# Performance work log

Measured on AMD Instinct MI355X. Metric: run time of the kernel, lower is better.

The kernel has to match this reference:

```python
import jax, jax.numpy as jnp
import numpy as np

B, T, IN, H, K = 128, 4096, 2, 64, 2  # batch, seq_len, input feat, lstm hidden, num tags


def setup_inputs() -> dict:
    key = jax.random.key(0)
    ks = jax.random.split(key, 16)
    s = 1.0 / np.sqrt(H)
    u = lambda k, shape, a: jax.random.uniform(k, shape, jnp.float32, -a, a)
    p = {}
    p['x'] = jax.random.normal(ks[0], (B, T, IN), jnp.float32)
    # layer 0 (input IN), layer 1 (input 2H); leading dim 2 = [forward, backward] direction
    p['w_ih0'] = u(ks[1], (2, 4 * H, IN), s)
    p['w_hh0'] = u(ks[2], (2, 4 * H, H), s)
    p['b_ih0'] = u(ks[3], (2, 4 * H), s)
    p['b_hh0'] = u(ks[4], (2, 4 * H), s)
    p['w_ih1'] = u(ks[5], (2, 4 * H, 2 * H), s)
    p['w_hh1'] = u(ks[6], (2, 4 * H, H), s)
    p['b_ih1'] = u(ks[7], (2, 4 * H), s)
    p['b_hh1'] = u(ks[8], (2, 4 * H), s)
    p['fc_w'] = u(ks[9], (K, 2 * H), 1.0 / np.sqrt(2 * H))
    p['fc_b'] = u(ks[10], (K,), 1.0 / np.sqrt(2 * H))
    # CRF params (torchcrf init: U(-0.1, 0.1))
    p['trans'] = u(ks[11], (K, K), 0.1)
    p['start'] = u(ks[12], (K,), 0.1)
    p['end'] = u(ks[13], (K,), 0.1)
    return p


def _lstm_dir(xg, w_hh, b_hh):
    # xg: [T, B, 4H] precomputed input projections; PyTorch gate order i, f, g, o
    b, h = xg.shape[1], w_hh.shape[1]

    def step(carry, g_x):
        hs, cs = carry
        g = g_x + hs @ w_hh.T + b_hh
        i, f, gg, o = jnp.split(g, 4, axis=-1)
        cs = jax.nn.sigmoid(f) * cs + jax.nn.sigmoid(i) * jnp.tanh(gg)
        hs = jax.nn.sigmoid(o) * jnp.tanh(cs)
        return (hs, cs), hs

    init = (jnp.zeros((b, h), xg.dtype), jnp.zeros((b, h), xg.dtype))
    _, out = jax.lax.scan(step, init, xg)
    return out  # [T, B, H]


def _bilstm_layer(xt, w_ih, w_hh, b_ih, b_hh):
    # xt: [T, B, F] time-major input
    xg_f = jnp.einsum('tbi,gi->tbg', xt, w_ih[0]) + b_ih[0]
    xg_b = jnp.einsum('tbi,gi->tbg', xt[::-1], w_ih[1]) + b_ih[1]
    hf = _lstm_dir(xg_f, w_hh[0], b_hh[0])
    hb = _lstm_dir(xg_b, w_hh[1], b_hh[1])[::-1]
    return jnp.concatenate([hf, hb], axis=-1)  # [T, B, 2H]


def _viterbi(logits, trans, start, end):
    # logits: [B, T, K] -> best path [B, T]
    e = jnp.swapaxes(logits, 0, 1)  # [T, B, K]
    score0 = start[None, :] + e[0]

    def fwd(score, e_t):
        cand = score[:, :, None] + trans[None, :, :]  # [B, Kprev, Knext]
        bp = jnp.argmax(cand, axis=1)
        return jnp.max(cand, axis=1) + e_t, bp

    score, bps = jax.lax.scan(fwd, score0, e[1:])  # bps: [T-1, B, K]
    last = jnp.argmax(score + end[None, :], axis=-1)  # [B]

    def back(tag, bp):
        prev = jnp.take_along_axis(bp, tag[:, None], axis=1)[:, 0]
        return prev, prev

    _, path = jax.lax.scan(back, last, bps, reverse=True)  # [T-1, B]
    return jnp.swapaxes(jnp.concatenate([path, last[None, :]], axis=0), 0, 1)


def reference(x, w_ih0, w_hh0, b_ih0, b_hh0, w_ih1, w_hh1, b_ih1, b_hh1,
              fc_w, fc_b, trans, start, end):
    xt = jnp.swapaxes(x, 0, 1)  # [T, B, IN]
    h0 = _bilstm_layer(xt, w_ih0, w_hh0, b_ih0, b_hh0)
    h1 = _bilstm_layer(h0, w_ih1, w_hh1, b_ih1, b_hh1)  # [T, B, 2H]
    logits = jnp.swapaxes(jnp.einsum('tbh,kh->tbk', h1, fc_w) + fc_b, 0, 1)  # [B, T, K]
    return _viterbi(logits, trans, start, end).astype(jnp.int32)
```

## Files before the change

kernel.cpp:

```cpp
#include <hip/hip_runtime.h>
#include <hip/hip_bf16.h>

#define TT 4096
#define BATCH 128
#define HID 64
#define CK 32
#define NCH (TT / CK)
#define NSLOT (NCH + 1)

__device__ __forceinline__ float sigm(float x) { return 1.f / (1.f + expf(-x)); }
__device__ __forceinline__ float tanh_f(float x) { float e = expf(2.f * x); return 1.f - 2.f / (e + 1.f); }

__global__ __launch_bounds__(256, 1) void lstm_ckpt(
    const float* __restrict__ x,
    const float* __restrict__ w_ih,
    const float* __restrict__ w_hh,
    const float* __restrict__ b_ih, const float* __restrict__ b_hh,
    float* __restrict__ ckpt)
{
    const int blk = blockIdx.x;
    const int dir = blk & 1;
    const int b   = blk >> 1;
    const int tid = threadIdx.x;

    __shared__ __align__(16) float xs[TT * 2];
    __shared__ __align__(16) float h_lds[HID];
    __shared__ __align__(16) float g_lds[256];

    {
        const float4* src = (const float4*)(x + (size_t)b * TT * 2);
        float4* dst = (float4*)xs;
        #pragma unroll
        for (int r = 0; r < 8; ++r) dst[tid + r * 256] = src[tid + r * 256];
    }
    const int row = dir * 256 + tid;
    float wv[HID];
    {
        const float4* wr = (const float4*)(w_hh + (size_t)row * HID);
        #pragma unroll
        for (int k = 0; k < 16; ++k) {
            float4 v = wr[k];
            wv[4*k] = v.x; wv[4*k+1] = v.y; wv[4*k+2] = v.z; wv[4*k+3] = v.w;
        }
    }
    const float wx0 = w_ih[row * 2 + 0], wx1 = w_ih[row * 2 + 1];
    const float bias = b_ih[row] + b_hh[row];
    const int gtype = tid >> 6;
    float c = 0.f, hreg = 0.f;
    if (tid < HID) h_lds[tid] = 0.f;
    __syncthreads();

    for (int t = 0; t < TT; ++t) {
        const int tt = dir ? (TT - 1 - t) : t;
        if (tid < HID) {
            const int bnum = dir ? (tt + 1) : tt;
            if ((bnum & (CK - 1)) == 0) {
                float* cp = ckpt + (((size_t)(dir * BATCH + b) * NSLOT + (bnum >> 5)) << 7);
                cp[tid] = hreg; cp[HID + tid] = c;
            }
        }
        const float base = bias + wx0 * xs[tt * 2] + wx1 * xs[tt * 2 + 1];
        float a0 = 0.f, a1 = 0.f, a2 = 0.f, a3 = 0.f;
        const float4* h4 = (const float4*)h_lds;
        #pragma unroll
        for (int k = 0; k < 16; ++k) {
            float4 hv = h4[k];
            a0 = fmaf(wv[4*k],   hv.x, a0);
            a1 = fmaf(wv[4*k+1], hv.y, a1);
            a2 = fmaf(wv[4*k+2], hv.z, a2);
            a3 = fmaf(wv[4*k+3], hv.w, a3);
        }
        const float acc = base + ((a0 + a1) + (a2 + a3));
        g_lds[tid] = (gtype == 2) ? tanh_f(acc) : sigm(acc);
        __syncthreads();
        if (tid < HID) {
            const float iv = g_lds[tid], fv = g_lds[64 + tid], gg = g_lds[128 + tid], ov = g_lds[192 + tid];
            c = fv * c + iv * gg;
            hreg = ov * tanh_f(c);
            h_lds[tid] = hreg;
        }
        __syncthreads();
    }
}

__global__ __launch_bounds__(1024) void lstm_fused1(
    const float* __restrict__ x,
    const float* __restrict__ w_ih0, const float* __restrict__ w_hh0,
    const float* __restrict__ b_ih0, const float* __restrict__ b_hh0,
    const float* __restrict__ w_ih1, const float* __restrict__ w_hh1,
    const float* __restrict__ b_ih1, const float* __restrict__ b_hh1,
    const float* __restrict__ fc_w,  const float* __restrict__ ckpt,
    float* __restrict__ plog)
{
    const int blk = blockIdx.x;
    const int l1dir = blk & 1;
    const int b = blk >> 1;
    const int tid = threadIdx.x;

    __shared__ __align__(16) float h0buf[2][CK][128];
    __shared__ __align__(16) float xbuf[2][CK][2];
    __shared__ __align__(16) float g1[256];
    __shared__ __align__(16) float g0[2][256];
    __shared__ __align__(16) float h1_lds[HID];
    __shared__ __align__(16) float h0s[2][HID];

    const bool isL1 = (tid < 512);
    const int l1row = tid >> 1;
    const int l1half = tid & 1;
    const int d0 = (tid >> 8) - 2;
    const int st0 = tid & 255;

    float wreg[96];
    float bias_, fw0 = 0.f, fw1 = 0.f;
    int gtype_;
    float c_state = 0.f, ckh = 0.f, ckc = 0.f;
    float4 xpre = make_float4(0.f, 0.f, 0.f, 0.f);

    if (isL1) {
        const int grow = l1dir * 256 + l1row;
        const float* wi = w_ih1 + (size_t)grow * 128;
        const float* wh = w_hh1 + (size_t)grow * 64;
        const float4* srcA = (const float4*)wi + (l1half ? 24 : 0);
        const float4* srcB = l1half ? (const float4*)wh : ((const float4*)wi + 8);
        #pragma unroll
        for (int k = 0; k < 8; ++k) {
            float4 v = srcA[k];
            wreg[4*k] = v.x; wreg[4*k+1] = v.y; wreg[4*k+2] = v.z; wreg[4*k+3] = v.w;
        }
        #pragma unroll
        for (int k = 0; k < 16; ++k) {
            float4 v = srcB[k];
            wreg[32+4*k] = v.x; wreg[32+4*k+1] = v.y; wreg[32+4*k+2] = v.z; wreg[32+4*k+3] = v.w;
        }
        bias_ = b_ih1[grow] + b_hh1[grow];
        gtype_ = l1row >> 6;
    } else {
        const int growd = d0 * 256 + st0;
        const float4* wh = (const float4*)(w_hh0 + (size_t)growd * 64);
        #pragma unroll
        for (int k = 0; k < 16; ++k) {
            float4 v = wh[k];
            wreg[4*k] = v.x; wreg[4*k+1] = v.y; wreg[4*k+2] = v.z; wreg[4*k+3] = v.w;
        }
        wreg[64] = w_ih0[growd * 2 + 0];
        wreg[65] = w_ih0[growd * 2 + 1];
        bias_ = b_ih0[growd] + b_hh0[growd];
        gtype_ = st0 >> 6;
        if (d0 == 1 && st0 >= 64 && st0 < 128) {
            fw0 = fc_w[l1dir * 64 + (st0 - 64)];
            fw1 = fc_w[128 + l1dir * 64 + (st0 - 64)];
        }
    }

    if (tid < HID) h1_lds[tid] = 0.f;
    {
        const int ch0 = l1dir ? (NCH - 1) : 0;
        if (tid < 16)
            ((float4*)xbuf[0])[tid] = ((const float4*)(x + ((size_t)b * TT + (size_t)ch0 * CK) * 2))[tid];
        if (!isL1 && st0 < HID) {
            const int slot = d0 ? (ch0 + 1) : ch0;
            const float* cp = ckpt + (((size_t)(d0 * BATCH + b) * NSLOT + slot) << 7);
            h0s[d0][st0] = cp[st0];
            c_state = cp[HID + st0];
        }
    }
    __syncthreads();

    auto stepf = [&](int s, int ml, int mc, int mp) {
        if (s == 0 && mp >= 0 && !isL1) {
            const int chp = l1dir ? (NCH - 1 - mp) : mp;
            if (st0 < HID) {
                const int slot = d0 ? (chp + 1) : chp;
                const float* cp = ckpt + (((size_t)(d0 * BATCH + b) * NSLOT + slot) << 7);
                ckh = cp[st0]; ckc = cp[HID + st0];
            }
            if (d0 == 1 && st0 >= 128 && st0 < 144)
                xpre = ((const float4*)(x + ((size_t)b * TT + (size_t)chp * CK) * 2))[st0 - 128];
        }
        if (isL1) {
            if (ml >= 0) {
                const int trow = l1dir ? (CK - 1 - s) : s;
                const float* h0row = h0buf[ml & 1][trow];
                const float4* pA = (const float4*)h0row + (l1half ? 24 : 0);
                const float4* pB = l1half ? (const float4*)h1_lds : ((const float4*)h0row + 8);
                float a0 = 0.f, a1 = 0.f, a2 = 0.f, a3 = 0.f;
                #pragma unroll
                for (int k = 0; k < 8; ++k) {
                    float4 v = pA[k];
                    a0 = fmaf(wreg[4*k],   v.x, a0);
                    a1 = fmaf(wreg[4*k+1], v.y, a1);
                    a2 = fmaf(wreg[4*k+2], v.z, a2);
                    a3 = fmaf(wreg[4*k+3], v.w, a3);
                }
                #pragma unroll
                for (int k = 0; k < 16; ++k) {
                    float4 v = pB[k];
                    a0 = fmaf(wreg[32+4*k],   v.x, a0);
                    a1 = fmaf(wreg[32+4*k+1], v.y, a1);
                    a2 = fmaf(wreg[32+4*k+2], v.z, a2);
                    a3 = fmaf(wreg[32+4*k+3], v.w, a3);
                }
                float tot = (a0 + a1) + (a2 + a3);
                tot += __shfl_xor(tot, 1);
                tot += bias_;
                const float gv = (gtype_ == 2) ? tanh_f(tot) : sigm(tot);
                if (l1half == 0) g1[l1row] = gv;
            }
        } else {
            if (mc >= 0) {
                const int r0 = d0 ? (CK - 1 - s) : s;
                const float4* hsrc = (const float4*)h0s[d0];
                float a0 = 0.f, a1 = 0.f, a2 = 0.f, a3 = 0.f;
                #pragma unroll
                for (int k = 0; k < 16; ++k) {
                    float4 v = hsrc[k];
                    a0 = fmaf(wreg[4*k],   v.x, a0);
                    a1 = fmaf(wreg[4*k+1], v.y, a1);
                    a2 = fmaf(wreg[4*k+2], v.z, a2);
                    a3 = fmaf(wreg[4*k+3], v.w, a3);
                }
                float tot = (a0 + a1) + (a2 + a3) + bias_
                          + wreg[64] * xbuf[mc & 1][r0][0] + wreg[65] * xbuf[mc & 1][r0][1];
                const float gv = (gtype_ == 2) ? tanh_f(tot) : sigm(tot);
                g0[d0][st0] = gv;
            }
            if (d0 == 1 && st0 >= 64 && st0 < 128 && ml >= 0) {
                const int gt = ml * CK + s;
                if (gt > 0) {
                    const int l = st0 - 64;
                    const float hv = h1_lds[l];
                    float p0 = hv * fw0, p1 = hv * fw1;
                    #pragma unroll
                    for (int d_ = 32; d_ > 0; d_ >>= 1) { p0 += __shfl_xor(p0, d_); p1 += __shfl_xor(p1, d_); }
                    if (l == 0) {
                        const int tp = l1dir ? (TT - gt) : (gt - 1);
                        *(float2*)(plog + (((size_t)l1dir * BATCH + b) * TT + tp) * 2) = make_float2(p0, p1);
                    }
                }
            }
        }
        __syncthreads();
        if (isL1) {
            if (ml >= 0 && tid < HID) {
                const float iv = g1[tid], fv = g1[64 + tid], gg = g1[128 + tid], ov = g1[192 + tid];
                c_state = fv * c_state + iv * gg;
                h1_lds[tid] = ov * tanh_f(c_state);
            }
        } else {
            if (mc >= 0 && st0 < HID) {
                const float iv = g0[d0][st0], fv = g0[d0][64 + st0], gg = g0[d0][128 + st0], ov = g0[d0][192 + st0];
                c_state = fv * c_state + iv * gg;
                const float hv = ov * tanh_f(c_state);
                const int orow = d0 ? (CK - 1 - s) : s;
                h0buf[mc & 1][orow][d0 * HID + st0] = hv;
                if (s == CK - 1 && mp >= 0) { h0s[d0][st0] = ckh; c_state = ckc; }
                else h0s[d0][st0] = hv;
            }
            if (s == CK - 1 && mp >= 0 && d0 == 1 && st0 >= 128 && st0 < 144)
                ((float4*)xbuf[mp & 1])[st0 - 128] = xpre;
        }
        __syncthreads();
    };

    for (int s = 0; s < CK; ++s) stepf(s, -1, 0, 1);
    for (int i = 0; i < NCH; ++i) {
        const int mc = (i + 1 < NCH) ? (i + 1) : -1;
        const int mp = (i + 2 < NCH) ? (i + 2) : -1;
        for (int s = 0; s < CK; ++s) stepf(s, i, mc, mp);
    }
    if (!isL1 && d0 == 1 && st0 >= 64 && st0 < 128) {
        const int l = st0 - 64;
        const float hv = h1_lds[l];
        float p0 = hv * fw0, p1 = hv * fw1;
        #pragma unroll
        for (int d_ = 32; d_ > 0; d_ >>= 1) { p0 += __shfl_xor(p0, d_); p1 += __shfl_xor(p1, d_); }
        if (l == 0) {
            const int tp = l1dir ? 0 : (TT - 1);
            *(float2*)(plog + (((size_t)l1dir * BATCH + b) * TT + tp) * 2) = make_float2(p0, p1);
        }
    }
}

__device__ __forceinline__ unsigned long long shfl_u64(unsigned long long v, int src) {
    unsigned int lo = (unsigned int)v, hi = (unsigned int)(v >> 32);
    lo = __shfl(lo, src); hi = __shfl(hi, src);
    return ((unsigned long long)hi << 32) | lo;
}

__global__ __launch_bounds__(64, 1) void viterbi_k(
    const float* __restrict__ plog, const float* __restrict__ fc_b,
    const float* __restrict__ trans, const float* __restrict__ startv,
    const float* __restrict__ endv, int* __restrict__ out)
{
    const int b = blockIdx.x;
    const int lane = threadIdx.x;
    __shared__ __align__(16) float2 e_lds[64][65];

    const float fb0 = fc_b[0], fb1 = fc_b[1];
    const float* pf = plog + ((size_t)(0 * BATCH + b) * TT) * 2;
    const float* pb = plog + ((size_t)(1 * BATCH + b) * TT) * 2;
    for (int r = 0; r < 32; ++r) {
        const int i4 = r * 64 + lane;
        float4 a = ((const float4*)pf)[i4];
        float4 cc = ((const float4*)pb)[i4];
        const int t0 = 2 * i4, t1 = t0 + 1;
        e_lds[t0 & 63][t0 >> 6] = make_float2(a.x + cc.x + fb0, a.y + cc.y + fb1);
        e_lds[t1 & 63][t1 >> 6] = make_float2(a.z + cc.z + fb0, a.w + cc.w + fb1);
    }
    __syncthreads();
    const float tr00 = trans[0], tr01 = trans[1], tr10 = trans[2], tr11 = trans[3];
    const float2 e0 = e_lds[0][0];
    const float s00 = startv[0] + e0.x, s01 = startv[1] + e0.y;

    const int lo = lane * 64;
    const int hi = (lane == 63) ? (TT - 1) : (lo + 64);
    float a00, a01, a10, a11;
    {
        const float2 ee = e_lds[(lo + 1) & 63][(lo + 1) >> 6];
        a00 = tr00 + ee.x; a01 = tr01 + ee.y; a10 = tr10 + ee.x; a11 = tr11 + ee.y;
    }
    for (int t = lo + 2; t <= hi; ++t) {
        const float2 ee = e_lds[t & 63][t >> 6];
        const float n00 = fmaxf(a00 + tr00, a01 + tr10) + ee.x;
        const float n01 = fmaxf(a00 + tr01, a01 + tr11) + ee.y;
        const float n10 = fmaxf(a10 + tr00, a11 + tr10) + ee.x;
        const float n11 = fmaxf(a10 + tr01, a11 + tr11) + ee.y;
        a00 = n00; a01 = n01; a10 = n10; a11 = n11;
    }
    #pragma unroll
    for (int d = 1; d < 64; d <<= 1) {
        const float o00 = __shfl_up(a00, d), o01 = __shfl_up(a01, d);
        const float o10 = __shfl_up(a10, d), o11 = __shfl_up(a11, d);
        if (lane >= d) {
            const float n00 = fmaxf(o00 + a00, o01 + a10);
            const float n01 = fmaxf(o00 + a01, o01 + a11);
            const float n10 = fmaxf(o10 + a00, o11 + a10);
            const float n11 = fmaxf(o10 + a01, o11 + a11);
            a00 = n00; a01 = n01; a10 = n10; a11 = n11;
        }
    }
    const float p00 = __shfl_up(a00, 1), p01 = __shfl_up(a01, 1);
    const float p10 = __shfl_up(a10, 1), p11 = __shfl_up(a11, 1);
    float s0, s1;
    if (lane == 0) { s0 = s00; s1 = s01; }
    else { s0 = fmaxf(s00 + p00, s01 + p10); s1 = fmaxf(s00 + p01, s01 + p11); }
    unsigned long long m0 = 0ull, m1 = 0ull;
    for (int t = lo + 1; t <= hi; ++t) {
        const float2 ee = e_lds[t & 63][t >> 6];
        const float c00 = s0 + tr00, c10 = s1 + tr10;
        const float c01 = s0 + tr01, c11 = s1 + tr11;
        const int bp0 = c10 > c00, bp1 = c11 > c01;
        s0 = (bp0 ? c10 : c00) + ee.x;
        s1 = (bp1 ? c11 : c01) + ee.y;
        m0 |= (unsigned long long)bp0 << (t - lo - 1);
        m1 |= (unsigned long long)bp1 << (t - lo - 1);
    }
    int last;
    {
        const int lt = (s1 + endv[1]) > (s0 + endv[0]);
        last = __shfl(lt, 63);
    }
    int f0 = 0, f1 = 1;
    for (int t = hi; t > lo; --t) {
        const int s_ = t - lo - 1;
        f0 = (int)(((f0 ? m1 : m0) >> s_) & 1ull);
        f1 = (int)(((f1 ? m1 : m0) >> s_) & 1ull);
    }
    int mm = f0 | (f1 << 1);
    #pragma unroll
    for (int d = 1; d < 64; d <<= 1) {
        const int mo = __shfl_down(mm, d);
        if (lane + d < 64) {
            const int r0 = (mm >> (mo & 1)) & 1;
            const int r1 = (mm >> ((mo >> 1) & 1)) & 1;
            mm = r0 | (r1 << 1);
        }
    }
    const int gn = __shfl_down(mm, 1);
    int cur = (lane == 63) ? last : ((gn >> last) & 1);
    unsigned long long tagm = 0ull;
    if (lane == 63) tagm |= (unsigned long long)last << 63;
    for (int t = hi; t > lo; --t) {
        const int s_ = t - lo - 1;
        cur = (int)(((cur ? m1 : m0) >> s_) & 1ull);
        tagm |= (unsigned long long)cur << s_;
    }
    int* ob = out + (size_t)b * TT;
    for (int r = 0; r < 64; ++r) {
        const unsigned long long mr = shfl_u64(tagm, r);
        ob[r * 64 + lane] = (int)((mr >> lane) & 1ull);
    }
}

extern "C" void kernel_launch(void* const* d_in, const int* in_sizes, int n_in,
                              void* d_out, int out_size, void* d_ws, size_t ws_size,
                              hipStream_t stream) {
    const float* x      = (const float*)d_in[0];
    const float* w_ih0  = (const float*)d_in[1];
    const float* w_hh0  = (const float*)d_in[2];
    const float* b_ih0  = (const float*)d_in[3];
    const float* b_hh0  = (const float*)d_in[4];
    const float* w_ih1  = (const float*)d_in[5];
    const float* w_hh1  = (const float*)d_in[6];
    const float* b_ih1  = (const float*)d_in[7];
    const float* b_hh1  = (const float*)d_in[8];
    const float* fc_w   = (const float*)d_in[9];
    const float* fc_b   = (const float*)d_in[10];
    const float* trans  = (const float*)d_in[11];
    const float* startv = (const float*)d_in[12];
    const float* endv   = (const float*)d_in[13];

    char* ws = (char*)d_ws;
    const size_t ckpt_bytes = (size_t)2 * BATCH * NSLOT * 128 * 4;
    float* ckpt = (float*)ws;
    float* plog = (float*)(ws + ckpt_bytes);

    lstm_ckpt<<<256, 256, 0, stream>>>(x, w_ih0, w_hh0, b_ih0, b_hh0, ckpt);
    lstm_fused1<<<256, 1024, 0, stream>>>(x, w_ih0, w_hh0, b_ih0, b_hh0,
                                          w_ih1, w_hh1, b_ih1, b_hh1,
                                          fc_w, ckpt, plog);
    viterbi_k<<<128, 64, 0, stream>>>(plog, fc_b, trans, startv, endv, (int*)d_out);
}
```

Before: 8.068 ms.

## Halve fused LSTM block to 512 threads with two gate rows per thread

```diff
diff --git a/kernel.cpp b/kernel.cpp
--- a/kernel.cpp
+++ b/kernel.cpp
@@ -83,7 +83,7 @@
     }
 }
 
-__global__ __launch_bounds__(1024) void lstm_fused1(
+__global__ __launch_bounds__(512, 2) void lstm_fused1(
     const float* __restrict__ x,
     const float* __restrict__ w_ih0, const float* __restrict__ w_hh0,
     const float* __restrict__ b_ih0, const float* __restrict__ b_hh0,
@@ -101,163 +101,169 @@
     __shared__ __align__(16) float xbuf[2][CK][2];
     __shared__ __align__(16) float g1[256];
     __shared__ __align__(16) float g0[2][256];
-    __shared__ __align__(16) float h1_lds[HID];
+    __shared__ __align__(16) float h1b[2][HID];
     __shared__ __align__(16) float h0s[2][HID];
 
-    const bool isL1 = (tid < 512);
-    const int l1row = tid >> 1;
-    const int l1half = tid & 1;
-    const int d0 = (tid >> 8) - 2;
-    const int st0 = tid & 255;
-
-    float wreg[96];
-    float bias_, fw0 = 0.f, fw1 = 0.f;
-    int gtype_;
-    float c_state = 0.f, ckh = 0.f, ckc = 0.f;
+    const bool isL1 = (tid < 256);
+    const int t0 = tid - 256;
+    const int dg = t0 >> 7;
+    const int jg = t0 & 127;
+    const int du = t0 >> 6;
+    const int eu = t0 & 63;
+
+    float wreg[192];
+    float bias0 = 0.f, bias1 = 0.f;
+    float fw0 = 0.f, fw1 = 0.f;
+    float c_st = 0.f;
+    float ckh = 0.f, ckc = 0.f;
     float4 xpre = make_float4(0.f, 0.f, 0.f, 0.f);
 
     if (isL1) {
-        const int grow = l1dir * 256 + l1row;
-        const float* wi = w_ih1 + (size_t)grow * 128;
-        const float* wh = w_hh1 + (size_t)grow * 64;
-        const float4* srcA = (const float4*)wi + (l1half ? 24 : 0);
-        const float4* srcB = l1half ? (const float4*)wh : ((const float4*)wi + 8);
-        #pragma unroll
-        for (int k = 0; k < 8; ++k) {
-            float4 v = srcA[k];
+        const int grow = l1dir * 256 + tid;
+        const float4* wia = (const float4*)(w_ih1 + (size_t)grow * 128);
+        #pragma unroll
+        for (int k = 0; k < 32; ++k) {
+            float4 v = wia[k];
             wreg[4*k] = v.x; wreg[4*k+1] = v.y; wreg[4*k+2] = v.z; wreg[4*k+3] = v.w;
         }
+        const float4* wha = (const float4*)(w_hh1 + (size_t)grow * 64);
         #pragma unroll
         for (int k = 0; k < 16; ++k) {
-            float4 v = srcB[k];
-            wreg[32+4*k] = v.x; wreg[32+4*k+1] = v.y; wreg[32+4*k+2] = v.z; wreg[32+4*k+3] = v.w;
-        }
-        bias_ = b_ih1[grow] + b_hh1[grow];
-        gtype_ = l1row >> 6;
+            float4 v = wha[k];
+            wreg[128+4*k] = v.x; wreg[128+4*k+1] = v.y; wreg[128+4*k+2] = v.z; wreg[128+4*k+3] = v.w;
+        }
+        bias0 = b_ih1[grow] + b_hh1[grow];
     } else {
-        const int growd = d0 * 256 + st0;
-        const float4* wh = (const float4*)(w_hh0 + (size_t)growd * 64);
+        const int rA = dg * 256 + jg;
+        const int rB = rA + 128;
+        const float4* wa = (const float4*)(w_hh0 + (size_t)rA * 64);
+        const float4* wb = (const float4*)(w_hh0 + (size_t)rB * 64);
         #pragma unroll
         for (int k = 0; k < 16; ++k) {
-            float4 v = wh[k];
+            float4 v = wa[k];
             wreg[4*k] = v.x; wreg[4*k+1] = v.y; wreg[4*k+2] = v.z; wreg[4*k+3] = v.w;
         }
-        wreg[64] = w_ih0[growd * 2 + 0];
-        wreg[65] = w_ih0[growd * 2 + 1];
-        bias_ = b_ih0[growd] + b_hh0[growd];
-        gtype_ = st0 >> 6;
-        if (d0 == 1 && st0 >= 64 && st0 < 128) {
-            fw0 = fc_w[l1dir * 64 + (st0 - 64)];
-            fw1 = fc_w[128 + l1dir * 64 + (st0 - 64)];
-        }
-    }
-
-    if (tid < HID) h1_lds[tid] = 0.f;
+        #pragma unroll
+        for (int k = 0; k < 16; ++k) {
+            float4 v = wb[k];
+            wreg[64+4*k] = v.x; wreg[64+4*k+1] = v.y; wreg[64+4*k+2] = v.z; wreg[64+4*k+3] = v.w;
+        }
+        wreg[128] = w_ih0[rA * 2 + 0]; wreg[129] = w_ih0[rA * 2 + 1];
+        wreg[130] = w_ih0[rB * 2 + 0]; wreg[131] = w_ih0[rB * 2 + 1];
+        bias0 = b_ih0[rA] + b_hh0[rA];
+        bias1 = b_ih0[rB] + b_hh0[rB];
+        if (t0 >= 128 && t0 < 192) {
+            fw0 = fc_w[l1dir * 64 + (t0 - 128)];
+            fw1 = fc_w[128 + l1dir * 64 + (t0 - 128)];
+        }
+    }
+
+    if (tid < HID) { h1b[0][tid] = 0.f; h1b[1][tid] = 0.f; }
     {
         const int ch0 = l1dir ? (NCH - 1) : 0;
-        if (tid < 16)
-            ((float4*)xbuf[0])[tid] = ((const float4*)(x + ((size_t)b * TT + (size_t)ch0 * CK) * 2))[tid];
-        if (!isL1 && st0 < HID) {
-            const int slot = d0 ? (ch0 + 1) : ch0;
-            const float* cp = ckpt + (((size_t)(d0 * BATCH + b) * NSLOT + slot) << 7);
-            h0s[d0][st0] = cp[st0];
-            c_state = cp[HID + st0];
+        if (!isL1 && t0 >= 192 && t0 < 208)
+            ((float4*)xbuf[0])[t0 - 192] = ((const float4*)(x + ((size_t)b * TT + (size_t)ch0 * CK) * 2))[t0 - 192];
+        if (!isL1 && t0 < 128) {
+            const int slot = du ? (ch0 + 1) : ch0;
+            const float* cp = ckpt + (((size_t)(du * BATCH + b) * NSLOT + slot) << 7);
+            h0s[du][eu] = cp[eu];
+            c_st = cp[HID + eu];
         }
     }
     __syncthreads();
 
     auto stepf = [&](int s, int ml, int mc, int mp) {
+        const int u = ml * CK + s;
         if (s == 0 && mp >= 0 && !isL1) {
             const int chp = l1dir ? (NCH - 1 - mp) : mp;
-            if (st0 < HID) {
-                const int slot = d0 ? (chp + 1) : chp;
-                const float* cp = ckpt + (((size_t)(d0 * BATCH + b) * NSLOT + slot) << 7);
-                ckh = cp[st0]; ckc = cp[HID + st0];
-            }
-            if (d0 == 1 && st0 >= 128 && st0 < 144)
-                xpre = ((const float4*)(x + ((size_t)b * TT + (size_t)chp * CK) * 2))[st0 - 128];
+            if (t0 < 128) {
+                const int slot = du ? (chp + 1) : chp;
+                const float* cp = ckpt + (((size_t)(du * BATCH + b) * NSLOT + slot) << 7);
+                ckh = cp[eu]; ckc = cp[HID + eu];
+            }
+            if (t0 >= 192 && t0 < 208)
+                xpre = ((const float4*)(x + ((size_t)b * TT + (size_t)chp * CK) * 2))[t0 - 192];
         }
         if (isL1) {
             if (ml >= 0) {
                 const int trow = l1dir ? (CK - 1 - s) : s;
-                const float* h0row = h0buf[ml & 1][trow];
-                const float4* pA = (const float4*)h0row + (l1half ? 24 : 0);
-                const float4* pB = l1half ? (const float4*)h1_lds : ((const float4*)h0row + 8);
+                const float4* p4 = (const float4*)h0buf[ml & 1][trow];
                 float a0 = 0.f, a1 = 0.f, a2 = 0.f, a3 = 0.f;
                 #pragma unroll
-                for (int k = 0; k < 8; ++k) {
-                    float4 v = pA[k];
+                for (int k = 0; k < 32; ++k) {
+                    float4 v = p4[k];
                     a0 = fmaf(wreg[4*k],   v.x, a0);
                     a1 = fmaf(wreg[4*k+1], v.y, a1);
                     a2 = fmaf(wreg[4*k+2], v.z, a2);
                     a3 = fmaf(wreg[4*k+3], v.w, a3);
                 }
+                const float4* h14 = (const float4*)h1b[u & 1];
                 #pragma unroll
                 for (int k = 0; k < 16; ++k) {
-                    float4 v = pB[k];
-                    a0 = fmaf(wreg[32+4*k],   v.x, a0);
-                    a1 = fmaf(wreg[32+4*k+1], v.y, a1);
-                    a2 = fmaf(wreg[32+4*k+2], v.z, a2);
-                    a3 = fmaf(wreg[32+4*k+3], v.w, a3);
+                    float4 v = h14[k];
+                    a0 = fmaf(wreg[128+4*k],   v.x, a0);
+                    a1 = fmaf(wreg[128+4*k+1], v.y, a1);
+                    a2 = fmaf(wreg[128+4*k+2], v.z, a2);
+                    a3 = fmaf(wreg[128+4*k+3], v.w, a3);
                 }
-                float tot = (a0 + a1) + (a2 + a3);
-                tot += __shfl_xor(tot, 1);
-                tot += bias_;
-                const float gv = (gtype_ == 2) ? tanh_f(tot) : sigm(tot);
-                if (l1half == 0) g1[l1row] = gv;
+                const float acc = bias0 + ((a0 + a1) + (a2 + a3));
+                g1[tid] = ((tid >> 6) == 2) ? tanh_f(acc) : sigm(acc);
+            }
+        } else if (mc >= 0) {
+            const int r0 = dg ? (CK - 1 - s) : s;
+            const float4* hp = (const float4*)h0s[dg];
+            float a0 = 0.f, a1 = 0.f, a2 = 0.f, a3 = 0.f;
+            float e0 = 0.f, e1 = 0.f, e2 = 0.f, e3 = 0.f;
+            #pragma unroll
+            for (int k = 0; k < 16; ++k) {
+                float4 v = hp[k];
+                a0 = fmaf(wreg[4*k],   v.x, a0);
+                a1 = fmaf(wreg[4*k+1], v.y, a1);
+                a2 = fmaf(wreg[4*k+2], v.z, a2);
+                a3 = fmaf(wreg[4*k+3], v.w, a3);
+                e0 = fmaf(wreg[64+4*k],   v.x, e0);
+                e1 = fmaf(wreg[64+4*k+1], v.y, e1);
+                e2 = fmaf(wreg[64+4*k+2], v.z, e2);
+                e3 = fmaf(wreg[64+4*k+3], v.w, e3);
+            }
+            const float xv0 = xbuf[mc & 1][r0][0], xv1 = xbuf[mc & 1][r0][1];
+            const float accA = bias0 + ((a0 + a1) + (a2 + a3)) + wreg[128] * xv0 + wreg[129] * xv1;
+            const float accB = bias1 + ((e0 + e1) + (e2 + e3)) + wreg[130] * xv0 + wreg[131] * xv1;
+            g0[dg][jg]       = sigm(accA);
+            g0[dg][jg + 128] = (jg < 64) ? tanh_f(accB) : sigm(accB);
+        }
+        __syncthreads();
+        if (isL1) {
+            if (ml >= 0 && tid < 64) {
+                const float iv = g1[tid], fv = g1[64 + tid], gg = g1[128 + tid], ov = g1[192 + tid];
+                c_st = fv * c_st + iv * gg;
+                h1b[(u + 1) & 1][tid] = ov * tanh_f(c_st);
             }
         } else {
-            if (mc >= 0) {
-                const int r0 = d0 ? (CK - 1 - s) : s;
-                const float4* hsrc = (const float4*)h0s[d0];
-                float a0 = 0.f, a1 = 0.f, a2 = 0.f, a3 = 0.f;
-                #pragma unroll
-                for (int k = 0; k < 16; ++k) {
-                    float4 v = hsrc[k];
-                    a0 = fmaf(wreg[4*k],   v.x, a0);
-                    a1 = fmaf(wreg[4*k+1], v.y, a1);
-                    a2 = fmaf(wreg[4*k+2], v.z, a2);
-                    a3 = fmaf(wreg[4*k+3], v.w, a3);
-                }
-                float tot = (a0 + a1) + (a2 + a3) + bias_
-                          + wreg[64] * xbuf[mc & 1][r0][0] + wreg[65] * xbuf[mc & 1][r0][1];
-                const float gv = (gtype_ == 2) ? tanh_f(tot) : sigm(tot);
-                g0[d0][st0] = gv;
-            }
-            if (d0 == 1 && st0 >= 64 && st0 < 128 && ml >= 0) {
-                const int gt = ml * CK + s;
-                if (gt > 0) {
-                    const int l = st0 - 64;
-                    const float hv = h1_lds[l];
+            if (mc >= 0 && t0 < 128) {
+                const float iv = g0[du][eu], fv = g0[du][64 + eu], gg = g0[du][128 + eu], ov = g0[du][192 + eu];
+                c_st = fv * c_st + iv * gg;
+                const float hv = ov * tanh_f(c_st);
+                const int orow = du ? (CK - 1 - s) : s;
+                h0buf[mc & 1][orow][du * 64 + eu] = hv;
+                if (s == CK - 1 && mp >= 0) { h0s[du][eu] = ckh; c_st = ckc; }
+                else h0s[du][eu] = hv;
+            }
+            if (ml >= 0 && t0 >= 128 && t0 < 192) {
+                if (u > 0) {
+                    const int l = t0 - 128;
+                    const float hv = h1b[u & 1][l];
                     float p0 = hv * fw0, p1 = hv * fw1;
                     #pragma unroll
                     for (int d_ = 32; d_ > 0; d_ >>= 1) { p0 += __shfl_xor(p0, d_); p1 += __shfl_xor(p1, d_); }
                     if (l == 0) {
-                        const int tp = l1dir ? (TT - gt) : (gt - 1);
+                        const int tp = l1dir ? (TT - u) : (u - 1);
                         *(float2*)(plog + (((size_t)l1dir * BATCH + b) * TT + tp) * 2) = make_float2(p0, p1);
                     }
                 }
             }
-        }
-        __syncthreads();
-        if (isL1) {
-            if (ml >= 0 && tid < HID) {
-                const float iv = g1[tid], fv = g1[64 + tid], gg = g1[128 + tid], ov = g1[192 + tid];
-                c_state = fv * c_state + iv * gg;
-                h1_lds[tid] = ov * tanh_f(c_state);
-            }
-        } else {
-            if (mc >= 0 && st0 < HID) {
-                const float iv = g0[d0][st0], fv = g0[d0][64 + st0], gg = g0[d0][128 + st0], ov = g0[d0][192 + st0];
-                c_state = fv * c_state + iv * gg;
-                const float hv = ov * tanh_f(c_state);
-                const int orow = d0 ? (CK - 1 - s) : s;
-                h0buf[mc & 1][orow][d0 * HID + st0] = hv;
-                if (s == CK - 1 && mp >= 0) { h0s[d0][st0] = ckh; c_state = ckc; }
-                else h0s[d0][st0] = hv;
-            }
-            if (s == CK - 1 && mp >= 0 && d0 == 1 && st0 >= 128 && st0 < 144)
-                ((float4*)xbuf[mp & 1])[st0 - 128] = xpre;
+            if (s == CK - 1 && mp >= 0 && t0 >= 192 && t0 < 208)
+                ((float4*)xbuf[mp & 1])[t0 - 192] = xpre;
         }
         __syncthreads();
     };
@@ -268,9 +274,9 @@
         const int mp = (i + 2 < NCH) ? (i + 2) : -1;
         for (int s = 0; s < CK; ++s) stepf(s, i, mc, mp);
     }
-    if (!isL1 && d0 == 1 && st0 >= 64 && st0 < 128) {
-        const int l = st0 - 64;
-        const float hv = h1_lds[l];
+    if (!isL1 && t0 >= 128 && t0 < 192) {
+        const int l = t0 - 128;
+        const float hv = h1b[0][l];
         float p0 = hv * fw0, p1 = hv * fw1;
         #pragma unroll
         for (int d_ = 32; d_ > 0; d_ >>= 1) { p0 += __shfl_xor(p0, d_); p1 += __shfl_xor(p1, d_); }
@@ -416,8 +422,8 @@
     float* plog = (float*)(ws + ckpt_bytes);
 
     lstm_ckpt<<<256, 256, 0, stream>>>(x, w_ih0, w_hh0, b_ih0, b_hh0, ckpt);
-    lstm_fused1<<<256, 1024, 0, stream>>>(x, w_ih0, w_hh0, b_ih0, b_hh0,
-                                          w_ih1, w_hh1, b_ih1, b_hh1,
-                                          fc_w, ckpt, plog);
+    lstm_fused1<<<256, 512, 0, stream>>>(x, w_ih0, w_hh0, b_ih0, b_hh0,
+                                         w_ih1, w_hh1, b_ih1, b_hh1,
+                                         fc_w, ckpt, plog);
     viterbi_k<<<128, 64, 0, stream>>>(plog, fc_b, trans, startv, endv, (int*)d_out);
 }
```

Result: slower. 11.63 ms (+44.2%).

## Add three-stage pipeline computing layer-1 input projections one chunk ahead

Applied to the files above, without the earlier changes.

```diff
diff --git a/kernel.cpp b/kernel.cpp
--- a/kernel.cpp
+++ b/kernel.cpp
@@ -1,5 +1,4 @@
 #include <hip/hip_runtime.h>
-#include <hip/hip_bf16.h>
 
 #define TT 4096
 #define BATCH 128
@@ -11,7 +10,7 @@
 __device__ __forceinline__ float sigm(float x) { return 1.f / (1.f + expf(-x)); }
 __device__ __forceinline__ float tanh_f(float x) { float e = expf(2.f * x); return 1.f - 2.f / (e + 1.f); }
 
-__global__ __launch_bounds__(256, 1) void lstm_ckpt(
+__global__ __launch_bounds__(512) __attribute__((amdgpu_waves_per_eu(2, 2))) void lstm_ckpt(
     const float* __restrict__ x,
     const float* __restrict__ w_ih,
     const float* __restrict__ w_hh,
@@ -22,6 +21,7 @@
     const int dir = blk & 1;
     const int b   = blk >> 1;
     const int tid = threadIdx.x;
+    const int row = tid >> 1, half = tid & 1;
 
     __shared__ __align__(16) float xs[TT * 2];
     __shared__ __align__(16) float h_lds[HID];
@@ -30,22 +30,22 @@
     {
         const float4* src = (const float4*)(x + (size_t)b * TT * 2);
         float4* dst = (float4*)xs;
-        #pragma unroll
-        for (int r = 0; r < 8; ++r) dst[tid + r * 256] = src[tid + r * 256];
-    }
-    const int row = dir * 256 + tid;
-    float wv[HID];
+        for (int rr = tid; rr < 2048; rr += 512) dst[rr] = src[rr];
+    }
+    const int grow = dir * 256 + row;
+    float wv[32];
     {
-        const float4* wr = (const float4*)(w_hh + (size_t)row * HID);
-        #pragma unroll
-        for (int k = 0; k < 16; ++k) {
+        const float4* wr = (const float4*)(w_hh + (size_t)grow * 64) + half * 8;
+        #pragma unroll
+        for (int k = 0; k < 8; ++k) {
             float4 v = wr[k];
             wv[4*k] = v.x; wv[4*k+1] = v.y; wv[4*k+2] = v.z; wv[4*k+3] = v.w;
         }
     }
-    const float wx0 = w_ih[row * 2 + 0], wx1 = w_ih[row * 2 + 1];
-    const float bias = b_ih[row] + b_hh[row];
-    const int gtype = tid >> 6;
+    const float wx0 = half ? 0.f : w_ih[grow * 2 + 0];
+    const float wx1 = half ? 0.f : w_ih[grow * 2 + 1];
+    const float bias = half ? 0.f : (b_ih[grow] + b_hh[grow]);
+    const int gtype = row >> 6;
     float c = 0.f, hreg = 0.f;
     if (tid < HID) h_lds[tid] = 0.f;
     __syncthreads();
@@ -59,19 +59,22 @@
                 cp[tid] = hreg; cp[HID + tid] = c;
             }
         }
-        const float base = bias + wx0 * xs[tt * 2] + wx1 * xs[tt * 2 + 1];
+        const float4* h4 = (const float4*)h_lds + half * 8;
         float a0 = 0.f, a1 = 0.f, a2 = 0.f, a3 = 0.f;
-        const float4* h4 = (const float4*)h_lds;
-        #pragma unroll
-        for (int k = 0; k < 16; ++k) {
+        #pragma unroll
+        for (int k = 0; k < 8; ++k) {
             float4 hv = h4[k];
             a0 = fmaf(wv[4*k],   hv.x, a0);
             a1 = fmaf(wv[4*k+1], hv.y, a1);
             a2 = fmaf(wv[4*k+2], hv.z, a2);
             a3 = fmaf(wv[4*k+3], hv.w, a3);
         }
-        const float acc = base + ((a0 + a1) + (a2 + a3));
-        g_lds[tid] = (gtype == 2) ? tanh_f(acc) : sigm(acc);
+        float tot = (a0 + a1) + (a2 + a3);
+        tot += __shfl_xor(tot, 1);
+        if (half == 0) {
+            const float acc = tot + bias + wx0 * xs[tt * 2] + wx1 * xs[tt * 2 + 1];
+            g_lds[row] = (gtype == 2) ? tanh_f(acc) : sigm(acc);
+        }
         __syncthreads();
         if (tid < HID) {
             const float iv = g_lds[tid], fv = g_lds[64 + tid], gg = g_lds[128 + tid], ov = g_lds[192 + tid];
@@ -83,7 +86,8 @@
     }
 }
 
-__global__ __launch_bounds__(1024) void lstm_fused1(
+__global__ __attribute__((amdgpu_flat_work_group_size(1024, 1024), amdgpu_waves_per_eu(4, 4)))
+void lstm_fused1(
     const float* __restrict__ x,
     const float* __restrict__ w_ih0, const float* __restrict__ w_hh0,
     const float* __restrict__ b_ih0, const float* __restrict__ b_hh0,
@@ -98,183 +102,184 @@
     const int tid = threadIdx.x;
 
     __shared__ __align__(16) float h0buf[2][CK][128];
+    __shared__ __align__(16) float xg1[2][CK][256];
     __shared__ __align__(16) float xbuf[2][CK][2];
     __shared__ __align__(16) float g1[256];
     __shared__ __align__(16) float g0[2][256];
-    __shared__ __align__(16) float h1_lds[HID];
+    __shared__ __align__(16) float h1b[2][HID];
     __shared__ __align__(16) float h0s[2][HID];
 
-    const bool isL1 = (tid < 512);
-    const int l1row = tid >> 1;
-    const int l1half = tid & 1;
-    const int d0 = (tid >> 8) - 2;
-    const int st0 = tid & 255;
-
-    float wreg[96];
-    float bias_, fw0 = 0.f, fw1 = 0.f;
-    int gtype_;
-    float c_state = 0.f, ckh = 0.f, ckc = 0.f;
+    const bool isL1 = tid < 256;
+    const bool isL0 = (tid >= 256) && (tid < 768);
+    const bool isG  = tid >= 768;
+    const int q0 = tid - 256;
+    const int d0 = (q0 >> 8) & 1;
+    const int j0 = q0 & 255;
+    const int jg = (tid - 768) & 255;
+
+    float r[64];
+    float bias_ = 0.f, wx0 = 0.f, wx1 = 0.f, fw0 = 0.f, fw1 = 0.f;
+    float c1 = 0.f, c0 = 0.f, ckh = 0.f, ckc = 0.f;
     float4 xpre = make_float4(0.f, 0.f, 0.f, 0.f);
+    float4 wc = make_float4(0.f, 0.f, 0.f, 0.f);
+    const float4* wip4 = (const float4*)(w_ih1 + (size_t)(l1dir * 256 + jg) * 128);
 
     if (isL1) {
-        const int grow = l1dir * 256 + l1row;
-        const float* wi = w_ih1 + (size_t)grow * 128;
-        const float* wh = w_hh1 + (size_t)grow * 64;
-        const float4* srcA = (const float4*)wi + (l1half ? 24 : 0);
-        const float4* srcB = l1half ? (const float4*)wh : ((const float4*)wi + 8);
-        #pragma unroll
-        for (int k = 0; k < 8; ++k) {
-            float4 v = srcA[k];
-            wreg[4*k] = v.x; wreg[4*k+1] = v.y; wreg[4*k+2] = v.z; wreg[4*k+3] = v.w;
-        }
+        const int grow = l1dir * 256 + tid;
+        const float4* wr = (const float4*)(w_hh1 + (size_t)grow * 64);
         #pragma unroll
         for (int k = 0; k < 16; ++k) {
-            float4 v = srcB[k];
-            wreg[32+4*k] = v.x; wreg[32+4*k+1] = v.y; wreg[32+4*k+2] = v.z; wreg[32+4*k+3] = v.w;
+            float4 v = wr[k];
+            r[4*k] = v.x; r[4*k+1] = v.y; r[4*k+2] = v.z; r[4*k+3] = v.w;
         }
         bias_ = b_ih1[grow] + b_hh1[grow];
-        gtype_ = l1row >> 6;
+        if (tid >= 64 && tid < 128) {
+            fw0 = fc_w[l1dir * 64 + (tid - 64)];
+            fw1 = fc_w[128 + l1dir * 64 + (tid - 64)];
+        }
+    } else if (isL0) {
+        const int grow = d0 * 256 + j0;
+        const float4* wr = (const float4*)(w_hh0 + (size_t)grow * 64);
+        #pragma unroll
+        for (int k = 0; k < 16; ++k) {
+            float4 v = wr[k];
+            r[4*k] = v.x; r[4*k+1] = v.y; r[4*k+2] = v.z; r[4*k+3] = v.w;
+        }
+        wx0 = w_ih0[grow * 2 + 0];
+        wx1 = w_ih0[grow * 2 + 1];
+        bias_ = b_ih0[grow] + b_hh0[grow];
     } else {
-        const int growd = d0 * 256 + st0;
-        const float4* wh = (const float4*)(w_hh0 + (size_t)growd * 64);
-        #pragma unroll
-        for (int k = 0; k < 16; ++k) {
-            float4 v = wh[k];
-            wreg[4*k] = v.x; wreg[4*k+1] = v.y; wreg[4*k+2] = v.z; wreg[4*k+3] = v.w;
-        }
-        wreg[64] = w_ih0[growd * 2 + 0];
-        wreg[65] = w_ih0[growd * 2 + 1];
-        bias_ = b_ih0[growd] + b_hh0[growd];
-        gtype_ = st0 >> 6;
-        if (d0 == 1 && st0 >= 64 && st0 < 128) {
-            fw0 = fc_w[l1dir * 64 + (st0 - 64)];
-            fw1 = fc_w[128 + l1dir * 64 + (st0 - 64)];
-        }
-    }
-
-    if (tid < HID) h1_lds[tid] = 0.f;
+        #pragma unroll
+        for (int k = 0; k < 32; ++k) r[k] = 0.f;
+        wc = wip4[0];
+    }
+
+    if (tid < HID) { h1b[0][tid] = 0.f; h1b[1][tid] = 0.f; }
     {
-        const int ch0 = l1dir ? (NCH - 1) : 0;
+        const int ac0 = l1dir ? (NCH - 1) : 0;
         if (tid < 16)
-            ((float4*)xbuf[0])[tid] = ((const float4*)(x + ((size_t)b * TT + (size_t)ch0 * CK) * 2))[tid];
-        if (!isL1 && st0 < HID) {
-            const int slot = d0 ? (ch0 + 1) : ch0;
+            ((float4*)xbuf[0])[tid] = ((const float4*)(x + ((size_t)b * TT + (size_t)ac0 * CK) * 2))[tid];
+        if (isL0 && j0 < 64) {
+            const int slot = d0 ? (ac0 + 1) : ac0;
             const float* cp = ckpt + (((size_t)(d0 * BATCH + b) * NSLOT + slot) << 7);
-            h0s[d0][st0] = cp[st0];
-            c_state = cp[HID + st0];
+            h0s[d0][j0] = cp[j0];
+            c0 = cp[HID + j0];
         }
     }
     __syncthreads();
 
-    auto stepf = [&](int s, int ml, int mc, int mp) {
-        if (s == 0 && mp >= 0 && !isL1) {
-            const int chp = l1dir ? (NCH - 1 - mp) : mp;
-            if (st0 < HID) {
-                const int slot = d0 ? (chp + 1) : chp;
-                const float* cp = ckpt + (((size_t)(d0 * BATCH + b) * NSLOT + slot) << 7);
-                ckh = cp[st0]; ckc = cp[HID + st0];
+    for (int i = -2; i < NCH; ++i) {
+        const bool l1act = i >= 0;
+        const bool gact  = (i + 1 >= 0) && (i + 1 < NCH);
+        const bool l0act = (i + 2) < NCH;
+        const int hbL0 = i & 1;
+        const int hbG  = (i + 1) & 1;
+        for (int s = 0; s < CK; ++s) {
+            if (isG) {
+                if (gact) {
+                    float4 wn = wip4[(s + 1) & (CK - 1)];
+                    const float4* hb = (const float4*)&h0buf[hbG][0][0] + s;
+                    #pragma unroll
+                    for (int s2 = 0; s2 < 32; ++s2) {
+                        float4 hv = hb[s2 * 32];
+                        float t0 = r[s2];
+                        t0 = fmaf(wc.x, hv.x, t0);
+                        t0 = fmaf(wc.y, hv.y, t0);
+                        t0 = fmaf(wc.z, hv.z, t0);
+                        t0 = fmaf(wc.w, hv.w, t0);
+                        r[s2] = t0;
+                    }
+                    if (s == CK - 1) {
+                        #pragma unroll
+                        for (int s2 = 0; s2 < 32; ++s2) { xg1[hbG][s2][jg] = r[s2]; r[s2] = 0.f; }
+                    }
+                    wc = wn;
+                }
+            } else if (isL0) {
+                if (s == 0 && j0 < 64 && (i + 3) < NCH) {
+                    const int acn = l1dir ? (NCH - 1 - (i + 3)) : (i + 3);
+                    const int slot = d0 ? (acn + 1) : acn;
+                    const float* cp = ckpt + (((size_t)(d0 * BATCH + b) * NSLOT + slot) << 7);
+                    ckh = cp[j0]; ckc = cp[HID + j0];
+                }
+                if (l0act) {
+                    const int orow = d0 ? (CK - 1 - s) : s;
+                    const float4* h4 = (const float4*)h0s[d0];
+                    float a0 = 0.f, a1 = 0.f, a2 = 0.f, a3 = 0.f;
+                    #pragma unroll
+                    for (int k = 0; k < 16; ++k) {
+                        float4 hv = h4[k];
+                        a0 = fmaf(r[4*k],   hv.x, a0);
+                        a1 = fmaf(r[4*k+1], hv.y, a1);
+                        a2 = fmaf(r[4*k+2], hv.z, a2);
+                        a3 = fmaf(r[4*k+3], hv.w, a3);
+                    }
+                    const float acc = bias_ + wx0 * xbuf[i & 1][orow][0] + wx1 * xbuf[i & 1][orow][1]
+                                    + ((a0 + a1) + (a2 + a3));
+                    g0[d0][j0] = ((j0 >> 6) == 2) ? tanh_f(acc) : sigm(acc);
+                }
+            } else {
+                if (s == 0 && tid >= 128 && tid < 144 && (i + 3) < NCH) {
+                    const int acn = l1dir ? (NCH - 1 - (i + 3)) : (i + 3);
+                    xpre = ((const float4*)(x + ((size_t)b * TT + (size_t)acn * CK) * 2))[tid - 128];
+                }
+                if (l1act) {
+                    const int u = i * CK + s;
+                    const float4* h4 = (const float4*)h1b[u & 1];
+                    float a0 = 0.f, a1 = 0.f, a2 = 0.f, a3 = 0.f;
+                    #pragma unroll
+                    for (int k = 0; k < 16; ++k) {
+                        float4 hv = h4[k];
+                        a0 = fmaf(r[4*k],   hv.x, a0);
+                        a1 = fmaf(r[4*k+1], hv.y, a1);
+                        a2 = fmaf(r[4*k+2], hv.z, a2);
+                        a3 = fmaf(r[4*k+3], hv.w, a3);
+                    }
+                    const int srow = l1dir ? (CK - 1 - s) : s;
+                    const float acc = bias_ + xg1[i & 1][srow][tid] + ((a0 + a1) + (a2 + a3));
+                    g1[tid] = ((tid >> 6) == 2) ? tanh_f(acc) : sigm(acc);
+                    if (tid >= 64 && tid < 128 && u > 0) {
+                        const float hv = h1b[u & 1][tid - 64];
+                        float p0 = hv * fw0, p1 = hv * fw1;
+                        #pragma unroll
+                        for (int d_ = 32; d_ > 0; d_ >>= 1) { p0 += __shfl_xor(p0, d_); p1 += __shfl_xor(p1, d_); }
+                        if (tid == 64) {
+                            const int tp = l1dir ? (TT - u) : (u - 1);
+                            *(float2*)(plog + (((size_t)l1dir * BATCH + b) * TT + tp) * 2) = make_float2(p0, p1);
+                        }
+                    }
+                }
             }
-            if (d0 == 1 && st0 >= 128 && st0 < 144)
-                xpre = ((const float4*)(x + ((size_t)b * TT + (size_t)chp * CK) * 2))[st0 - 128];
-        }
-        if (isL1) {
-            if (ml >= 0) {
-                const int trow = l1dir ? (CK - 1 - s) : s;
-                const float* h0row = h0buf[ml & 1][trow];
-                const float4* pA = (const float4*)h0row + (l1half ? 24 : 0);
-                const float4* pB = l1half ? (const float4*)h1_lds : ((const float4*)h0row + 8);
-                float a0 = 0.f, a1 = 0.f, a2 = 0.f, a3 = 0.f;
-                #pragma unroll
-                for (int k = 0; k < 8; ++k) {
-                    float4 v = pA[k];
-                    a0 = fmaf(wreg[4*k],   v.x, a0);
-                    a1 = fmaf(wreg[4*k+1], v.y, a1);
-                    a2 = fmaf(wreg[4*k+2], v.z, a2);
-                    a3 = fmaf(wreg[4*k+3], v.w, a3);
-                }
-                #pragma unroll
-                for (int k = 0; k < 16; ++k) {
-                    float4 v = pB[k];
-                    a0 = fmaf(wreg[32+4*k],   v.x, a0);
-                    a1 = fmaf(wreg[32+4*k+1], v.y, a1);
-                    a2 = fmaf(wreg[32+4*k+2], v.z, a2);
-                    a3 = fmaf(wreg[32+4*k+3], v.w, a3);
-                }
-                float tot = (a0 + a1) + (a2 + a3);
-                tot += __shfl_xor(tot, 1);
-                tot += bias_;
-                const float gv = (gtype_ == 2) ? tanh_f(tot) : sigm(tot);
-                if (l1half == 0) g1[l1row] = gv;
+            __syncthreads();
+            if (isL1) {
+                if (l1act && tid < 64) {
+                    const int u = i * CK + s;
+                    const float iv = g1[tid], fv = g1[64 + tid], gg = g1[128 + tid], ov = g1[192 + tid];
+                    c1 = fv * c1 + iv * gg;
+                    h1b[(u + 1) & 1][tid] = ov * tanh_f(c1);
+                }
+                if (s == CK - 1 && tid >= 128 && tid < 144 && (i + 3) < NCH)
+                    ((float4*)xbuf[(i + 1) & 1])[tid - 128] = xpre;
+            } else if (isL0) {
+                if (l0act && j0 < 64) {
+                    const float iv = g0[d0][j0], fv = g0[d0][64 + j0], gg = g0[d0][128 + j0], ov = g0[d0][192 + j0];
+                    c0 = fv * c0 + iv * gg;
+                    const float hv = ov * tanh_f(c0);
+                    const int orow = d0 ? (CK - 1 - s) : s;
+                    h0buf[hbL0][orow][d0 * 64 + j0] = hv;
+                    if (s == CK - 1 && (i + 3) < NCH) { h0s[d0][j0] = ckh; c0 = ckc; }
+                    else h0s[d0][j0] = hv;
+                }
             }
-        } else {
-            if (mc >= 0) {
-                const int r0 = d0 ? (CK - 1 - s) : s;
-                const float4* hsrc = (const float4*)h0s[d0];
-                float a0 = 0.f, a1 = 0.f, a2 = 0.f, a3 = 0.f;
-                #pragma unroll
-                for (int k = 0; k < 16; ++k) {
-                    float4 v = hsrc[k];
-                    a0 = fmaf(wreg[4*k],   v.x, a0);
-                    a1 = fmaf(wreg[4*k+1], v.y, a1);
-                    a2 = fmaf(wreg[4*k+2], v.z, a2);
-                    a3 = fmaf(wreg[4*k+3], v.w, a3);
-                }
-                float tot = (a0 + a1) + (a2 + a3) + bias_
-                          + wreg[64] * xbuf[mc & 1][r0][0] + wreg[65] * xbuf[mc & 1][r0][1];
-                const float gv = (gtype_ == 2) ? tanh_f(tot) : sigm(tot);
-                g0[d0][st0] = gv;
-            }
-            if (d0 == 1 && st0 >= 64 && st0 < 128 && ml >= 0) {
-                const int gt = ml * CK + s;
-                if (gt > 0) {
-                    const int l = st0 - 64;
-                    const float hv = h1_lds[l];
-                    float p0 = hv * fw0, p1 = hv * fw1;
-                    #pragma unroll
-                    for (int d_ = 32; d_ > 0; d_ >>= 1) { p0 += __shfl_xor(p0, d_); p1 += __shfl_xor(p1, d_); }
-                    if (l == 0) {
-                        const int tp = l1dir ? (TT - gt) : (gt - 1);
-                        *(float2*)(plog + (((size_t)l1dir * BATCH + b) * TT + tp) * 2) = make_float2(p0, p1);
-                    }
-                }
-            }
-        }
-        __syncthreads();
-        if (isL1) {
-            if (ml >= 0 && tid < HID) {
-                const float iv = g1[tid], fv = g1[64 + tid], gg = g1[128 + tid], ov = g1[192 + tid];
-                c_state = fv * c_state + iv * gg;
-                h1_lds[tid] = ov * tanh_f(c_state);
-            }
-        } else {
-            if (mc >= 0 && st0 < HID) {
-                const float iv = g0[d0][st0], fv = g0[d0][64 + st0], gg = g0[d0][128 + st0], ov = g0[d0][192 + st0];
-                c_state = fv * c_state + iv * gg;
-                const float hv = ov * tanh_f(c_state);
-                const int orow = d0 ? (CK - 1 - s) : s;
-                h0buf[mc & 1][orow][d0 * HID + st0] = hv;
-                if (s == CK - 1 && mp >= 0) { h0s[d0][st0] = ckh; c_state = ckc; }
-                else h0s[d0][st0] = hv;
-            }
-            if (s == CK - 1 && mp >= 0 && d0 == 1 && st0 >= 128 && st0 < 144)
-                ((float4*)xbuf[mp & 1])[st0 - 128] = xpre;
-        }
-        __syncthreads();
-    };
-
-    for (int s = 0; s < CK; ++s) stepf(s, -1, 0, 1);
-    for (int i = 0; i < NCH; ++i) {
-        const int mc = (i + 1 < NCH) ? (i + 1) : -1;
-        const int mp = (i + 2 < NCH) ? (i + 2) : -1;
-        for (int s = 0; s < CK; ++s) stepf(s, i, mc, mp);
-    }
-    if (!isL1 && d0 == 1 && st0 >= 64 && st0 < 128) {
-        const int l = st0 - 64;
-        const float hv = h1_lds[l];
+            __syncthreads();
+        }
+    }
+    if (isL1 && tid >= 64 && tid < 128) {
+        const float hv = h1b[0][tid - 64];
         float p0 = hv * fw0, p1 = hv * fw1;
         #pragma unroll
         for (int d_ = 32; d_ > 0; d_ >>= 1) { p0 += __shfl_xor(p0, d_); p1 += __shfl_xor(p1, d_); }
-        if (l == 0) {
+        if (tid == 64) {
             const int tp = l1dir ? 0 : (TT - 1);
             *(float2*)(plog + (((size_t)l1dir * BATCH + b) * TT + tp) * 2) = make_float2(p0, p1);
         }
@@ -415,7 +420,7 @@
     float* ckpt = (float*)ws;
     float* plog = (float*)(ws + ckpt_bytes);
 
-    lstm_ckpt<<<256, 256, 0, stream>>>(x, w_ih0, w_hh0, b_ih0, b_hh0, ckpt);
+    lstm_ckpt<<<256, 512, 0, stream>>>(x, w_ih0, w_hh0, b_ih0, b_hh0, ckpt);
     lstm_fused1<<<256, 1024, 0, stream>>>(x, w_ih0, w_hh0, b_ih0, b_hh0,
                                           w_ih1, w_hh1, b_ih1, b_hh1,
                                           fc_w, ckpt, plog);
```

Result: slower. 8.276 ms (+2.6%).
